# Optimization experiments

Hardware: AMD Instinct MI355X
Metric: run time of the kernel (lower is better)

Reference implementation:

```python
import jax, jax.numpy as jnp
import numpy as np

N = 100000        # nodes
E = 3200000       # edges (avg degree 32)
F_IN = 512        # input node features
HIDDEN = 16       # hardcoded in GCN.__init__
NUM_CLASSES = 40


def setup_inputs() -> dict:
    key = jax.random.key(0)
    k1, k2, k3, k4 = jax.random.split(key, 4)
    edge_index = jax.random.randint(k1, (2, E), 0, N, dtype=jnp.int32)
    x = jax.random.normal(k2, (N, F_IN), dtype=jnp.float32)
    # GCNConv weights (glorot-ish scale) and biases
    W1 = jax.random.normal(k3, (F_IN, HIDDEN), dtype=jnp.float32) * (1.0 / np.sqrt(F_IN))
    b1 = jnp.zeros((HIDDEN,), dtype=jnp.float32)
    W2 = jax.random.normal(k4, (HIDDEN, NUM_CLASSES), dtype=jnp.float32) * (1.0 / np.sqrt(HIDDEN))
    b2 = jnp.zeros((NUM_CLASSES,), dtype=jnp.float32)
    return {"edge_index": edge_index, "x": x, "W1": W1, "b1": b1, "W2": W2, "b2": b2}


def _gcn_conv(x, src, dst, W, b, n):
    # PyG GCNConv: linear transform, symmetric-normalized scatter-add aggregation
    h = x @ W                                             # [N, out]
    deg = jax.ops.segment_sum(jnp.ones_like(dst, dtype=h.dtype), dst, num_segments=n)
    dinv = jnp.where(deg > 0, jax.lax.rsqrt(deg), 0.0)    # deg^{-1/2}
    norm = dinv[src] * dinv[dst]                          # [E_total]
    out = jax.ops.segment_sum(h[src] * norm[:, None], dst, num_segments=n)
    return out + b


def reference(edge_index, x, W1, b1, W2, b2):
    n = x.shape[0]
    # GCNConv adds self-loops by default
    loop = jnp.arange(n, dtype=edge_index.dtype)
    src = jnp.concatenate([edge_index[0], loop])
    dst = jnp.concatenate([edge_index[1], loop])
    h = _gcn_conv(x, src, dst, W1, b1, n)
    h = jax.nn.relu(h)
    # F.dropout(training=self.training) -> identity in eval mode
    h = _gcn_conv(h, src, dst, W2, b2, n)
    return jax.nn.log_softmax(h, axis=1)[::20]
```

## Files before the change

### kernel.cpp

```cpp
#include <hip/hip_runtime.h>
#include <hip/hip_bf16.h>
#include <cstdint>
#include <math.h>

#define F_IN 512
#define HID  16
#define NCLS 40
#define OUT_STRIDE 20
#define TB   256
#define NBA  256
#define CAP  16384

typedef __attribute__((ext_vector_type(8))) short short8;
typedef __attribute__((ext_vector_type(4))) float f32x4;

__device__ inline unsigned short f2bf(float f) {
    unsigned u = __float_as_uint(f);
    u += 0x7fff + ((u >> 16) & 1);
    return (unsigned short)(u >> 16);
}
__device__ inline float bf2f(unsigned v) {
    return __uint_as_float(v << 16);
}

__global__ __launch_bounds__(256) void k_part(const int* __restrict__ src,
                                              const int* __restrict__ dst,
                                              int* __restrict__ gcnt,
                                              unsigned* __restrict__ bin,
                                              const float* __restrict__ W1,
                                              uint4* __restrict__ bfragg,
                                              int E, int NB, int chunk) {
    int t = threadIdx.x, blk = blockIdx.x;
    if (blk >= NBA) {
        int idx = (blk - NBA) * 256 + t;
        int kstep = idx >> 6, ln = idx & 63;
        int col = ln & 15, k0 = kstep * 32 + (ln >> 4) * 8;
        unsigned up[4];
#pragma unroll
        for (int i = 0; i < 4; i++) {
            float a = W1[(k0 + 2 * i) * HID + col];
            float b = W1[(k0 + 2 * i + 1) * HID + col];
            up[i] = (unsigned)f2bf(a) | ((unsigned)f2bf(b) << 16);
        }
        bfragg[idx] = make_uint4(up[0], up[1], up[2], up[3]);
        return;
    }
    __shared__ int h[512];
    __shared__ int pos[512];
    for (int b = t; b < NB; b += 256) h[b] = 0;
    __syncthreads();
    int e0 = blk * chunk, e1 = min(E, e0 + chunk);
    int nvec = (e1 - e0) >> 2;
    const int4* d4 = (const int4*)(dst + e0);
    const int4* s4 = (const int4*)(src + e0);
    for (int i = t; i < nvec; i += 256) {
        int4 d = d4[i];
        atomicAdd(&h[d.x >> 8], 1);
        atomicAdd(&h[d.y >> 8], 1);
        atomicAdd(&h[d.z >> 8], 1);
        atomicAdd(&h[d.w >> 8], 1);
    }
    for (int e = e0 + nvec * 4 + t; e < e1; e += 256)
        atomicAdd(&h[dst[e] >> 8], 1);
    __syncthreads();
    for (int b = t; b < NB; b += 256) {
        int c = h[b];
        int rb = c ? atomicAdd(&gcnt[b], c) : 0;
        pos[b] = b * CAP + rb;
    }
    __syncthreads();
    for (int i = t; i < nvec; i += 256) {
        int4 d = d4[i];
        int4 s = s4[i];
        int p;
        p = atomicAdd(&pos[d.x >> 8], 1); bin[p] = ((unsigned)s.x << 8) | (unsigned)(d.x & (TB - 1));
        p = atomicAdd(&pos[d.y >> 8], 1); bin[p] = ((unsigned)s.y << 8) | (unsigned)(d.y & (TB - 1));
        p = atomicAdd(&pos[d.z >> 8], 1); bin[p] = ((unsigned)s.z << 8) | (unsigned)(d.z & (TB - 1));
        p = atomicAdd(&pos[d.w >> 8], 1); bin[p] = ((unsigned)s.w << 8) | (unsigned)(d.w & (TB - 1));
    }
    for (int e = e0 + nvec * 4 + t; e < e1; e += 256) {
        int d = dst[e], s = src[e];
        int p = atomicAdd(&pos[d >> 8], 1);
        bin[p] = ((unsigned)s << 8) | (unsigned)(d & (TB - 1));
    }
}

__global__ __launch_bounds__(256) void k_sortb(const unsigned* __restrict__ bin,
                                               const int* __restrict__ gcnt,
                                               int* __restrict__ csr,
                                               int2* __restrict__ rng,
                                               float* __restrict__ dinv, int N) {
    __shared__ int cnt[TB], incl[TB], pos[TB];
    int t = threadIdx.x, b = blockIdx.x;
    cnt[t] = 0;
    __syncthreads();
    int j0 = b * CAP, count = gcnt[b];
    for (int j = t; j < count; j += 256)
        atomicAdd(&cnt[bin[j0 + j] & (TB - 1)], 1);
    __syncthreads();
    incl[t] = cnt[t];
    __syncthreads();
    for (int off = 1; off < TB; off <<= 1) {
        int v = (t >= off) ? incl[t - off] : 0;
        __syncthreads();
        incl[t] += v;
        __syncthreads();
    }
    int ex = incl[t] - cnt[t];
    pos[t] = ex;
    int node = b * TB + t;
    if (node < N) {
        rng[node] = make_int2(j0 + ex, j0 + ex + cnt[t]);
        dinv[node] = rsqrtf((float)cnt[t] + 1.0f);
    }
    __syncthreads();
    for (int j = t; j < count; j += 256) {
        unsigned v = bin[j0 + j];
        int p = atomicAdd(&pos[v & (TB - 1)], 1);
        csr[j0 + p] = (int)(v >> 8);
    }
}

__global__ __launch_bounds__(64) void k_gemm1m(const float* __restrict__ x,
                                               const uint4* __restrict__ bfragg,
                                               const float* __restrict__ dinv,
                                               unsigned short* __restrict__ h1b, int n) {
    __shared__ uint4 bl[16 * 64];
    int lane = threadIdx.x;
    for (int i = lane; i < 16 * 64; i += 64) bl[i] = bfragg[i];
    __syncthreads();

    int rows0 = blockIdx.x * 64;
    int arow = lane & 15, kgrp = lane >> 4;

    const float* xr[4];
#pragma unroll
    for (int rt = 0; rt < 4; rt++) {
        int r = rows0 + rt * 16 + arow;
        if (r >= n) r = n - 1;
        xr[rt] = x + (size_t)r * F_IN + kgrp * 8;
    }

    f32x4 acc[4];
#pragma unroll
    for (int rt = 0; rt < 4; rt++) acc[rt] = (f32x4){0.f, 0.f, 0.f, 0.f};

#pragma unroll 4
    for (int kstep = 0; kstep < 16; kstep++) {
        uint4 braw = bl[kstep * 64 + lane];
        short8 b;
        *(uint4*)&b = braw;
#pragma unroll
        for (int rt = 0; rt < 4; rt++) {
            f32x4 lo = __builtin_nontemporal_load((const f32x4*)(xr[rt] + kstep * 32));
            f32x4 hi = __builtin_nontemporal_load((const f32x4*)(xr[rt] + kstep * 32 + 4));
            __hip_bfloat162 c0 = __float22bfloat162_rn(make_float2(lo[0], lo[1]));
            __hip_bfloat162 c1 = __float22bfloat162_rn(make_float2(lo[2], lo[3]));
            __hip_bfloat162 c2 = __float22bfloat162_rn(make_float2(hi[0], hi[1]));
            __hip_bfloat162 c3 = __float22bfloat162_rn(make_float2(hi[2], hi[3]));
            uint4 araw;
            __builtin_memcpy(&araw.x, &c0, 4);
            __builtin_memcpy(&araw.y, &c1, 4);
            __builtin_memcpy(&araw.z, &c2, 4);
            __builtin_memcpy(&araw.w, &c3, 4);
            short8 a;
            *(uint4*)&a = araw;
            acc[rt] = __builtin_amdgcn_mfma_f32_16x16x32_bf16(a, b, acc[rt], 0, 0, 0);
        }
    }

    int col = lane & 15, rbase = (lane >> 4) * 4;
#pragma unroll
    for (int rt = 0; rt < 4; rt++) {
#pragma unroll
        for (int r = 0; r < 4; r++) {
            int row = rows0 + rt * 16 + rbase + r;
            if (row < n)
                h1b[(size_t)row * HID + col] = f2bf(acc[rt][r] * dinv[row]);
        }
    }
}

__global__ __launch_bounds__(256) void k_agg(const uint2* __restrict__ h1u2,
                                             const int* __restrict__ csr,
                                             const int2* __restrict__ rng,
                                             const float* __restrict__ dinv,
                                             const float* __restrict__ b1,
                                             uint2* __restrict__ zu2, int n) {
    int lane = threadIdx.x & 63;
    int wave0 = (blockIdx.x * blockDim.x + threadIdx.x) >> 6;
    int nwaves = (gridDim.x * blockDim.x) >> 6;
    int c2 = lane & 3;
    int sub = lane >> 2;
    float bl0 = b1[4 * c2 + 0], bl1 = b1[4 * c2 + 1];
    float bl2 = b1[4 * c2 + 2], bl3 = b1[4 * c2 + 3];
    for (int node = wave0; node < n; node += nwaves) {
        int2 r = rng[node];
        int s0 = r.x, s1 = r.y;
        uint2 us = h1u2[(size_t)node * 4 + c2];
        float s[4] = {0.f, 0.f, 0.f, 0.f};
        int j = s0 + sub;
        int nxt = (j < s1) ? __builtin_nontemporal_load(&csr[j]) : 0;
        for (; j < s1; j += 16) {
            int cur = nxt;
            int jn = j + 16;
            if (jn < s1) nxt = __builtin_nontemporal_load(&csr[jn]);
            uint2 u = h1u2[(size_t)cur * 4 + c2];
            s[0] += bf2f(u.x & 0xffff); s[1] += bf2f(u.x >> 16);
            s[2] += bf2f(u.y & 0xffff); s[3] += bf2f(u.y >> 16);
        }
#pragma unroll
        for (int m = 4; m < 64; m <<= 1) {
            s[0] += __shfl_xor(s[0], m); s[1] += __shfl_xor(s[1], m);
            s[2] += __shfl_xor(s[2], m); s[3] += __shfl_xor(s[3], m);
        }
        s[0] += bf2f(us.x & 0xffff); s[1] += bf2f(us.x >> 16);
        s[2] += bf2f(us.y & 0xffff); s[3] += bf2f(us.y >> 16);
        float dv = dinv[node];
        float p0 = dv * s[0] + bl0;
        float p1 = dv * s[1] + bl1;
        float p2 = dv * s[2] + bl2;
        float p3 = dv * s[3] + bl3;
        if (lane < 4) {
            uint2 o;
            o.x = (unsigned)f2bf(fmaxf(p0, 0.f) * dv) | ((unsigned)f2bf(fmaxf(p1, 0.f) * dv) << 16);
            o.y = (unsigned)f2bf(fmaxf(p2, 0.f) * dv) | ((unsigned)f2bf(fmaxf(p3, 0.f) * dv) << 16);
            zu2[(size_t)node * 4 + c2] = o;
        }
    }
}

__global__ void k_out(const unsigned short* __restrict__ zb,
                      const int* __restrict__ csr, const int2* __restrict__ rng,
                      const float* __restrict__ dinv, const float* __restrict__ W2,
                      const float* __restrict__ b2, float* __restrict__ out, int nOut) {
    int lane = threadIdx.x & 63;
    int wv = (blockIdx.x * blockDim.x + threadIdx.x) >> 6;
    if (wv >= nOut) return;
    int node = wv * OUT_STRIDE;
    int c = lane & 15, sub = lane >> 4;
    int2 r = rng[node];
    int s0 = r.x, s1 = r.y;
    float sum = 0.f;
    for (int j = s0 + sub; j < s1; j += 4)
        sum += bf2f(zb[(size_t)__builtin_nontemporal_load(&csr[j]) * HID + c]);
    sum += __shfl_xor(sum, 16);
    sum += __shfl_xor(sum, 32);
    sum += bf2f(zb[(size_t)node * HID + c]);
    float a = dinv[node] * sum;

    int jj = lane < NCLS ? lane : 0;
    float v = 0.f;
#pragma unroll
    for (int cc = 0; cc < 16; cc++) {
        float ac = __shfl(a, cc);
        v = fmaf(ac, W2[cc * NCLS + jj], v);
    }
    v += b2[jj];

    float vm = lane < NCLS ? v : -INFINITY;
    for (int off = 1; off < 64; off <<= 1) vm = fmaxf(vm, __shfl_xor(vm, off));
    float ex = lane < NCLS ? expf(v - vm) : 0.f;
    float se = ex;
    for (int off = 1; off < 64; off <<= 1) se += __shfl_xor(se, off);
    float ls = logf(se);
    if (lane < NCLS) out[(size_t)wv * NCLS + lane] = v - vm - ls;
}

extern "C" void kernel_launch(void* const* d_in, const int* in_sizes, int n_in,
                              void* d_out, int out_size, void* d_ws, size_t ws_size,
                              hipStream_t stream) {
    const int E = in_sizes[0] / 2;
    const int N = in_sizes[1] / F_IN;
    const int nOut = (N + OUT_STRIDE - 1) / OUT_STRIDE;
    const int NB = (N + TB - 1) / TB;
    const int chunk = (E + NBA - 1) / NBA;

    const int* src = (const int*)d_in[0];
    const int* dst = src + E;
    const float* x  = (const float*)d_in[1];
    const float* W1 = (const float*)d_in[2];
    const float* b1 = (const float*)d_in[3];
    const float* W2 = (const float*)d_in[4];
    const float* b2 = (const float*)d_in[5];
    float* out = (float*)d_out;

    uint8_t* w = (uint8_t*)d_ws;
    size_t off = 0;
    auto carve = [&](size_t bytes) {
        void* p = w + off;
        off += (bytes + 15) & ~(size_t)15;
        return p;
    };
    float*          dinv  = (float*)carve((size_t)N * 4);
    int*            gcnt  = (int*)carve((size_t)NB * 4);
    unsigned*       bin   = (unsigned*)carve((size_t)NB * CAP * 4);
    int*            csr   = (int*)carve((size_t)NB * CAP * 4);
    int2*           rng   = (int2*)carve((size_t)N * 8);
    unsigned short* h1b   = (unsigned short*)carve((size_t)N * HID * 2);
    unsigned short* zb    = (unsigned short*)carve((size_t)N * HID * 2);
    uint4*          bfragg= (uint4*)carve((size_t)16 * 64 * 16);
    (void)ws_size; (void)n_in; (void)out_size;

    (void)hipMemsetAsync(gcnt, 0, (size_t)NB * 4, stream);
    k_part <<<NBA + 4, 256, 0, stream>>>(src, dst, gcnt, bin, W1, bfragg, E, NB, chunk);
    k_sortb<<<NB, TB, 0, stream>>>(bin, gcnt, csr, rng, dinv, N);
    k_gemm1m<<<(N + 63) / 64, 64, 0, stream>>>(x, bfragg, dinv, h1b, N);
    k_agg  <<<2048, 256, 0, stream>>>((const uint2*)h1b, csr, rng, dinv, b1, (uint2*)zb, N);
    k_out  <<<(nOut * 64 + 255) / 256, 256, 0, stream>>>(zb, csr, rng, dinv, W2, b2, out, nOut);
}
```

Before: 172.8 us.

## Merge dense GEMM with edge partitioning into one launch, defer dinv scaling

The x@W1 MFMA GEMM now runs in the same launch as the edge-partition blocks, so the bandwidth-heavy read of x overlaps with the atomic-heavy binning instead of waiting until after the sort. The GEMM therefore writes unscaled h1, and the sort kernel rescales each node's row by dinv once the degree is known. This adds a read-modify-write pass over h1 and a second bf16 rounding, and each GEMM block now rebuilds the W1 fragments itself. The chunk size is also rounded to a multiple of 4.

```diff
diff --git a/kernel.cpp b/kernel.cpp
--- a/kernel.cpp
+++ b/kernel.cpp
@@ -23,30 +23,89 @@
     return __uint_as_float(v << 16);
 }
 
-__global__ __launch_bounds__(256) void k_part(const int* __restrict__ src,
-                                              const int* __restrict__ dst,
-                                              int* __restrict__ gcnt,
-                                              unsigned* __restrict__ bin,
-                                              const float* __restrict__ W1,
-                                              uint4* __restrict__ bfragg,
-                                              int E, int NB, int chunk) {
-    int t = threadIdx.x, blk = blockIdx.x;
-    if (blk >= NBA) {
-        int idx = (blk - NBA) * 256 + t;
-        int kstep = idx >> 6, ln = idx & 63;
-        int col = ln & 15, k0 = kstep * 32 + (ln >> 4) * 8;
-        unsigned up[4];
-#pragma unroll
-        for (int i = 0; i < 4; i++) {
-            float a = W1[(k0 + 2 * i) * HID + col];
-            float b = W1[(k0 + 2 * i + 1) * HID + col];
-            up[i] = (unsigned)f2bf(a) | ((unsigned)f2bf(b) << 16);
-        }
-        bfragg[idx] = make_uint4(up[0], up[1], up[2], up[3]);
+__global__ __launch_bounds__(256) void k_mega1(const float* __restrict__ x,
+                                               const float* __restrict__ W1,
+                                               unsigned short* __restrict__ h1b,
+                                               const int* __restrict__ src,
+                                               const int* __restrict__ dst,
+                                               int* __restrict__ gcnt,
+                                               unsigned* __restrict__ bin,
+                                               int E, int NB, int chunk,
+                                               int n, int GB) {
+    __shared__ uint4 bl[16 * 64];
+    int t = threadIdx.x;
+
+    if ((int)blockIdx.x < GB) {
+        for (int f = t; f < 16 * 64; f += 256) {
+            int kstep = f >> 6, ln = f & 63;
+            int col = ln & 15, k0 = kstep * 32 + (ln >> 4) * 8;
+            unsigned up[4];
+#pragma unroll
+            for (int i = 0; i < 4; i++) {
+                float a = W1[(k0 + 2 * i) * HID + col];
+                float b = W1[(k0 + 2 * i + 1) * HID + col];
+                up[i] = (unsigned)f2bf(a) | ((unsigned)f2bf(b) << 16);
+            }
+            bl[f] = make_uint4(up[0], up[1], up[2], up[3]);
+        }
+        __syncthreads();
+
+        int wid = t >> 6, lane = t & 63;
+        int rows0 = blockIdx.x * 256 + wid * 64;
+        int arow = lane & 15, kgrp = lane >> 4;
+
+        const float* xr[4];
+#pragma unroll
+        for (int rt = 0; rt < 4; rt++) {
+            int r = rows0 + rt * 16 + arow;
+            if (r >= n) r = n - 1;
+            xr[rt] = x + (size_t)r * F_IN + kgrp * 8;
+        }
+
+        f32x4 acc[4];
+#pragma unroll
+        for (int rt = 0; rt < 4; rt++) acc[rt] = (f32x4){0.f, 0.f, 0.f, 0.f};
+
+#pragma unroll 4
+        for (int kstep = 0; kstep < 16; kstep++) {
+            uint4 braw = bl[kstep * 64 + lane];
+            short8 b;
+            *(uint4*)&b = braw;
+#pragma unroll
+            for (int rt = 0; rt < 4; rt++) {
+                f32x4 lo = __builtin_nontemporal_load((const f32x4*)(xr[rt] + kstep * 32));
+                f32x4 hi = __builtin_nontemporal_load((const f32x4*)(xr[rt] + kstep * 32 + 4));
+                __hip_bfloat162 c0 = __float22bfloat162_rn(make_float2(lo[0], lo[1]));
+                __hip_bfloat162 c1 = __float22bfloat162_rn(make_float2(lo[2], lo[3]));
+                __hip_bfloat162 c2 = __float22bfloat162_rn(make_float2(hi[0], hi[1]));
+                __hip_bfloat162 c3 = __float22bfloat162_rn(make_float2(hi[2], hi[3]));
+                uint4 araw;
+                __builtin_memcpy(&araw.x, &c0, 4);
+                __builtin_memcpy(&araw.y, &c1, 4);
+                __builtin_memcpy(&araw.z, &c2, 4);
+                __builtin_memcpy(&araw.w, &c3, 4);
+                short8 a;
+                *(uint4*)&a = araw;
+                acc[rt] = __builtin_amdgcn_mfma_f32_16x16x32_bf16(a, b, acc[rt], 0, 0, 0);
+            }
+        }
+
+        int col = lane & 15, rbase = (lane >> 4) * 4;
+#pragma unroll
+        for (int rt = 0; rt < 4; rt++) {
+#pragma unroll
+            for (int r = 0; r < 4; r++) {
+                int row = rows0 + rt * 16 + rbase + r;
+                if (row < n)
+                    h1b[(size_t)row * HID + col] = f2bf(acc[rt][r]);
+            }
+        }
         return;
     }
-    __shared__ int h[512];
-    __shared__ int pos[512];
+
+    int blk = blockIdx.x - GB;
+    int* h = (int*)bl;
+    int* pos = h + 512;
     for (int b = t; b < NB; b += 256) h[b] = 0;
     __syncthreads();
     int e0 = blk * chunk, e1 = min(E, e0 + chunk);
@@ -85,11 +144,13 @@
     }
 }
 
-__global__ __launch_bounds__(256) void k_sortb(const unsigned* __restrict__ bin,
-                                               const int* __restrict__ gcnt,
-                                               int* __restrict__ csr,
-                                               int2* __restrict__ rng,
-                                               float* __restrict__ dinv, int N) {
+__global__ __launch_bounds__(256) void k_sortb2(const unsigned* __restrict__ bin,
+                                                const int* __restrict__ gcnt,
+                                                int* __restrict__ csr,
+                                                int2* __restrict__ rng,
+                                                float* __restrict__ dinv,
+                                                unsigned short* __restrict__ h1b,
+                                                int N) {
     __shared__ int cnt[TB], incl[TB], pos[TB];
     int t = threadIdx.x, b = blockIdx.x;
     cnt[t] = 0;
@@ -109,75 +170,27 @@
     int ex = incl[t] - cnt[t];
     pos[t] = ex;
     int node = b * TB + t;
+    float dv = rsqrtf((float)cnt[t] + 1.0f);
     if (node < N) {
         rng[node] = make_int2(j0 + ex, j0 + ex + cnt[t]);
-        dinv[node] = rsqrtf((float)cnt[t] + 1.0f);
+        dinv[node] = dv;
+        uint4* p = (uint4*)(h1b + (size_t)node * HID);
+        uint4 lo = p[0], hi = p[1];
+        unsigned w[8] = {lo.x, lo.y, lo.z, lo.w, hi.x, hi.y, hi.z, hi.w};
+#pragma unroll
+        for (int i = 0; i < 8; i++) {
+            float a = bf2f(w[i] & 0xffff) * dv;
+            float c = bf2f(w[i] >> 16) * dv;
+            w[i] = (unsigned)f2bf(a) | ((unsigned)f2bf(c) << 16);
+        }
+        p[0] = make_uint4(w[0], w[1], w[2], w[3]);
+        p[1] = make_uint4(w[4], w[5], w[6], w[7]);
     }
     __syncthreads();
     for (int j = t; j < count; j += 256) {
         unsigned v = bin[j0 + j];
-        int p = atomicAdd(&pos[v & (TB - 1)], 1);
-        csr[j0 + p] = (int)(v >> 8);
-    }
-}
-
-__global__ __launch_bounds__(64) void k_gemm1m(const float* __restrict__ x,
-                                               const uint4* __restrict__ bfragg,
-                                               const float* __restrict__ dinv,
-                                               unsigned short* __restrict__ h1b, int n) {
-    __shared__ uint4 bl[16 * 64];
-    int lane = threadIdx.x;
-    for (int i = lane; i < 16 * 64; i += 64) bl[i] = bfragg[i];
-    __syncthreads();
-
-    int rows0 = blockIdx.x * 64;
-    int arow = lane & 15, kgrp = lane >> 4;
-
-    const float* xr[4];
-#pragma unroll
-    for (int rt = 0; rt < 4; rt++) {
-        int r = rows0 + rt * 16 + arow;
-        if (r >= n) r = n - 1;
-        xr[rt] = x + (size_t)r * F_IN + kgrp * 8;
-    }
-
-    f32x4 acc[4];
-#pragma unroll
-    for (int rt = 0; rt < 4; rt++) acc[rt] = (f32x4){0.f, 0.f, 0.f, 0.f};
-
-#pragma unroll 4
-    for (int kstep = 0; kstep < 16; kstep++) {
-        uint4 braw = bl[kstep * 64 + lane];
-        short8 b;
-        *(uint4*)&b = braw;
-#pragma unroll
-        for (int rt = 0; rt < 4; rt++) {
-            f32x4 lo = __builtin_nontemporal_load((const f32x4*)(xr[rt] + kstep * 32));
-            f32x4 hi = __builtin_nontemporal_load((const f32x4*)(xr[rt] + kstep * 32 + 4));
-            __hip_bfloat162 c0 = __float22bfloat162_rn(make_float2(lo[0], lo[1]));
-            __hip_bfloat162 c1 = __float22bfloat162_rn(make_float2(lo[2], lo[3]));
-            __hip_bfloat162 c2 = __float22bfloat162_rn(make_float2(hi[0], hi[1]));
-            __hip_bfloat162 c3 = __float22bfloat162_rn(make_float2(hi[2], hi[3]));
-            uint4 araw;
-            __builtin_memcpy(&araw.x, &c0, 4);
-            __builtin_memcpy(&araw.y, &c1, 4);
-            __builtin_memcpy(&araw.z, &c2, 4);
-            __builtin_memcpy(&araw.w, &c3, 4);
-            short8 a;
-            *(uint4*)&a = araw;
-            acc[rt] = __builtin_amdgcn_mfma_f32_16x16x32_bf16(a, b, acc[rt], 0, 0, 0);
-        }
-    }
-
-    int col = lane & 15, rbase = (lane >> 4) * 4;
-#pragma unroll
-    for (int rt = 0; rt < 4; rt++) {
-#pragma unroll
-        for (int r = 0; r < 4; r++) {
-            int row = rows0 + rt * 16 + rbase + r;
-            if (row < n)
-                h1b[(size_t)row * HID + col] = f2bf(acc[rt][r] * dinv[row]);
-        }
+        int pp = atomicAdd(&pos[v & (TB - 1)], 1);
+        csr[j0 + pp] = (int)(v >> 8);
     }
 }
 
@@ -274,7 +287,8 @@
     const int N = in_sizes[1] / F_IN;
     const int nOut = (N + OUT_STRIDE - 1) / OUT_STRIDE;
     const int NB = (N + TB - 1) / TB;
-    const int chunk = (E + NBA - 1) / NBA;
+    const int chunk = ((E + NBA - 1) / NBA + 3) & ~3;
+    const int GB = (N + 255) / 256;
 
     const int* src = (const int*)d_in[0];
     const int* dst = src + E;
@@ -299,13 +313,12 @@
     int2*           rng   = (int2*)carve((size_t)N * 8);
     unsigned short* h1b   = (unsigned short*)carve((size_t)N * HID * 2);
     unsigned short* zb    = (unsigned short*)carve((size_t)N * HID * 2);
-    uint4*          bfragg= (uint4*)carve((size_t)16 * 64 * 16);
     (void)ws_size; (void)n_in; (void)out_size;
 
     (void)hipMemsetAsync(gcnt, 0, (size_t)NB * 4, stream);
-    k_part <<<NBA + 4, 256, 0, stream>>>(src, dst, gcnt, bin, W1, bfragg, E, NB, chunk);
-    k_sortb<<<NB, TB, 0, stream>>>(bin, gcnt, csr, rng, dinv, N);
-    k_gemm1m<<<(N + 63) / 64, 64, 0, stream>>>(x, bfragg, dinv, h1b, N);
+    k_mega1<<<GB + NBA, 256, 0, stream>>>(x, W1, h1b, src, dst, gcnt, bin,
+                                          E, NB, chunk, N, GB);
+    k_sortb2<<<NB, TB, 0, stream>>>(bin, gcnt, csr, rng, dinv, h1b, N);
     k_agg  <<<2048, 256, 0, stream>>>((const uint2*)h1b, csr, rng, dinv, b1, (uint2*)zb, N);
     k_out  <<<(nOut * 64 + 255) / 256, 256, 0, stream>>>(zb, csr, rng, dinv, W2, b2, out, nOut);
 }
```

New measurement: 171.9 us, median of 2. No clear change (-0.5%).
